# Kernel tuning notes

Measured on AMD Instinct MI355X. Metric: run time of the kernel, lower is better.

## Reference

```python
import jax, jax.numpy as jnp
import numpy as np

N = 50000      # nodes
E = 800000     # edges (avg degree 16)
F_IN = 128
H = 128
C = 2
EPS = 1e-5


def setup_inputs() -> dict:
    key = jax.random.key(0)
    ks = jax.random.split(key, 16)
    s_in = 1.0 / np.sqrt(F_IN)
    s_h = 1.0 / np.sqrt(H)
    return {
        "x": jax.random.normal(ks[0], (N, F_IN), jnp.float32),
        "edge_index": jax.random.randint(ks[1], (2, E), 0, N, jnp.int32),
        "W1": jax.random.normal(ks[2], (F_IN, H), jnp.float32) * s_in,
        "b1": jnp.zeros((H,), jnp.float32),
        "g1": jax.random.uniform(ks[3], (H,), jnp.float32, 0.5, 1.5),
        "be1": jnp.zeros((H,), jnp.float32),
        "m1": jax.random.normal(ks[4], (H,), jnp.float32) * 0.1,
        "v1": jax.random.uniform(ks[5], (H,), jnp.float32, 0.5, 1.5),
        "W2": jax.random.normal(ks[6], (H, H), jnp.float32) * s_h,
        "b2": jnp.zeros((H,), jnp.float32),
        "g2": jax.random.uniform(ks[7], (H,), jnp.float32, 0.5, 1.5),
        "be2": jnp.zeros((H,), jnp.float32),
        "m2": jax.random.normal(ks[8], (H,), jnp.float32) * 0.1,
        "v2": jax.random.uniform(ks[9], (H,), jnp.float32, 0.5, 1.5),
        "Wc": jax.random.normal(ks[10], (H, C), jnp.float32) * s_h,
        "bc": jnp.zeros((C,), jnp.float32),
    }


def _gcn_norm(edge_index):
    # Add self-loops: A_tilde = A + I, then symmetric normalization D^-1/2 A_tilde D^-1/2.
    loop = jnp.arange(N, dtype=edge_index.dtype)
    src = jnp.concatenate([edge_index[0], loop])
    dst = jnp.concatenate([edge_index[1], loop])
    deg = jax.ops.segment_sum(jnp.ones_like(src, jnp.float32), dst, num_segments=N)
    dinv = jnp.where(deg > 0, jax.lax.rsqrt(jnp.maximum(deg, 1.0)), 0.0)
    norm = dinv[src] * dinv[dst]  # per-edge coefficient
    return src, dst, norm


def _gcn_conv(h, src, dst, norm, W, b):
    h = h @ W                                  # [N, H]
    msg = h[src] * norm[:, None]               # gather + scale, [E+N, H]
    out = jax.ops.segment_sum(msg, dst, num_segments=N)
    return out + b


def _bn_eval(h, g, be, m, v):
    return (h - m) * (g * jax.lax.rsqrt(v + EPS)) + be


def reference(x, edge_index, W1, b1, g1, be1, m1, v1,
              W2, b2, g2, be2, m2, v2, Wc, bc):
    src, dst, norm = _gcn_norm(edge_index)
    h = _gcn_conv(x, src, dst, norm, W1, b1)
    h = jax.nn.relu(_bn_eval(h, g1, be1, m1, v1))  # dropout is identity in eval
    h = _gcn_conv(h, src, dst, norm, W2, b2)
    h = jax.nn.relu(_bn_eval(h, g2, be2, m2, v2))
    return h @ Wc + bc                            # logits [N, 2]
```

## Files before the change

kernel.cpp:

```cpp
#include <hip/hip_runtime.h>
#include <hip/hip_fp16.h>

#define EPSV 1e-5f
#define HSZ 6400
#define BPB 32

using half8 = __attribute__((ext_vector_type(8))) _Float16;
using f32x4 = __attribute__((ext_vector_type(4))) float;

__device__ __forceinline__ int bin_lo(int b, int mul) {
    return (int)((((long long)b << 25) + mul - 1) / mul);
}

__global__ __launch_bounds__(128) void k_setup(const float* __restrict__ W1, const float* __restrict__ W2,
                                               _Float16* __restrict__ whi1, _Float16* __restrict__ wlo1,
                                               _Float16* __restrict__ whi2, _Float16* __restrict__ wlo2,
                                               const float* __restrict__ g1, const float* __restrict__ v1,
                                               const float* __restrict__ b1, const float* __restrict__ m1,
                                               const float* __restrict__ be1,
                                               const float* __restrict__ g2, const float* __restrict__ v2,
                                               const float* __restrict__ b2, const float* __restrict__ m2,
                                               const float* __restrict__ be2,
                                               float* __restrict__ par, int* __restrict__ bcur) {
    int b = blockIdx.x;
    int t = threadIdx.x;
    if (b < 32) {
        const float* W = (b < 16) ? W1 : W2;
        _Float16* whi = (b < 16) ? whi1 : whi2;
        _Float16* wlo = (b < 16) ? wlo1 : wlo2;
        int tile = ((b & 15) << 1) | (t >> 6);
        int l = t & 63;
        int kt = tile >> 3, ct = tile & 7;
        int k0 = kt * 32 + (l >> 4) * 8;
        int c = ct * 16 + (l & 15);
        half8 hi, lo;
#pragma unroll
        for (int j = 0; j < 8; j++) {
            float w = W[(k0 + j) * 128 + c];
            _Float16 h = (_Float16)w;
            hi[j] = h;
            lo[j] = (_Float16)(w - (float)h);
        }
        size_t o = (size_t)tile * 64 + l;
        ((half8*)whi)[o] = hi;
        ((half8*)wlo)[o] = lo;
    } else {
        int c = t;
        float s1 = g1[c] * rsqrtf(v1[c] + EPSV);
        par[c] = s1;
        par[128 + c] = fmaf(b1[c] - m1[c], s1, be1[c]);
        float s2 = g2[c] * rsqrtf(v2[c] + EPSV);
        par[256 + c] = s2;
        par[384 + c] = fmaf(b2[c] - m2[c], s2, be2[c]);
        if (c < 8) bcur[c] = 0;
    }
}

__device__ __forceinline__ void bin_body(const int* __restrict__ src, const int* __restrict__ dst,
                                         int* __restrict__ bcur, unsigned int* __restrict__ binned,
                                         int E, int mul, int bin_cap, int bid, int nblocks, int tid) {
    int lane = tid & 63;
    int gw = (bid * 256 + tid) >> 6;
    int nw = (nblocks * 256) >> 6;
    bool v4 = ((E & 3) == 0);
    for (int base = gw * 1024; base < E; base += nw * 1024) {
        unsigned int vals[16];
        int bins[16];
        unsigned long long clo = 0, chi = 0;
#pragma unroll
        for (int g = 0; g < 4; g++) {
            int e0 = base + g * 256 + lane * 4;
            int4 s4, d4;
            if (v4 && e0 + 3 < E) {
                s4 = *(const int4*)(src + e0);
                d4 = *(const int4*)(dst + e0);
            } else {
                s4.x = (e0 < E) ? src[e0] : 0;         d4.x = (e0 < E) ? dst[e0] : -1;
                s4.y = (e0 + 1 < E) ? src[e0 + 1] : 0; d4.y = (e0 + 1 < E) ? dst[e0 + 1] : -1;
                s4.z = (e0 + 2 < E) ? src[e0 + 2] : 0; d4.z = (e0 + 2 < E) ? dst[e0 + 2] : -1;
                s4.w = (e0 + 3 < E) ? src[e0 + 3] : 0; d4.w = (e0 + 3 < E) ? dst[e0 + 3] : -1;
            }
            int ss[4] = {s4.x, s4.y, s4.z, s4.w};
            int dd[4] = {d4.x, d4.y, d4.z, d4.w};
#pragma unroll
            for (int k = 0; k < 4; k++) {
                int j = g * 4 + k;
                int d = dd[k];
                if (d >= 0) {
                    vals[j] = ((unsigned int)ss[k] << 16) | (unsigned int)d;
                    int b = (d * mul) >> 25;
                    bins[j] = b;
                    if (b < 4) clo += 1ull << (b * 16);
                    else       chi += 1ull << ((b - 4) * 16);
                } else bins[j] = -1;
            }
        }
        unsigned long long ilo = clo, ihi = chi;
#pragma unroll
        for (int d = 1; d < 64; d <<= 1) {
            unsigned long long ulo = __shfl_up(ilo, d, 64);
            unsigned long long uhi = __shfl_up(ihi, d, 64);
            if (lane >= d) { ilo += ulo; ihi += uhi; }
        }
        unsigned long long tlo = __shfl(ilo, 63, 64), thi = __shfl(ihi, 63, 64);
        unsigned long long plo = ilo - clo, phi = ihi - chi;
        int mytot = 0;
        if (lane < 4) mytot = (int)((tlo >> (lane * 16)) & 0xffff);
        else if (lane < 8) mytot = (int)((thi >> ((lane - 4) * 16)) & 0xffff);
        int alloc = 0;
        if (lane < 8) alloc = atomicAdd(&bcur[lane], mytot);
#pragma unroll
        for (int j = 0; j < 16; j++) {
            int b = bins[j];
            int bs = (b < 0) ? 0 : b;
            int bbase = __shfl(alloc, bs, 64);
            int sh = (bs & 3) * 16;
            unsigned long long sel = (bs < 4) ? plo : phi;
            int rel = (int)((sel >> sh) & 0xffffu);
            unsigned long long inc = 1ull << sh;
            if (bs < 4) plo += inc; else phi += inc;
            if (b >= 0) binned[(size_t)bs * bin_cap + bbase + rel] = vals[j];
        }
    }
}

template <bool AFP16>
__device__ __forceinline__ void gemm_body(const void* __restrict__ Araw,
                                          const _Float16* __restrict__ whi,
                                          const _Float16* __restrict__ wlo,
                                          unsigned short* __restrict__ out, int M,
                                          int bid, int tid, uint4* __restrict__ sB) {
    int l = tid & 63;
    int w = tid >> 6;
    int r0 = bid * 64 + w * 16;
    int ra = r0 + (l & 15);
    if (ra >= M) ra = M - 1;
    int kl = (l >> 4) * 8;

    half8 avh[4];
    float4 af0[4], af1[4];
    if constexpr (AFP16) {
#pragma unroll
        for (int kt = 0; kt < 4; kt++)
            avh[kt] = *(const half8*)((const _Float16*)Araw + (size_t)ra * 128 + kt * 32 + kl);
    } else {
#pragma unroll
        for (int kt = 0; kt < 4; kt++) {
            const float* pa = (const float*)Araw + (size_t)ra * 128 + kt * 32 + kl;
            af0[kt] = *(const float4*)pa;
            af1[kt] = *(const float4*)(pa + 4);
        }
    }

    {
        const uint4* gh = (const uint4*)whi;
        const uint4* gl = (const uint4*)wlo;
#pragma unroll
        for (int i = 0; i < 8; i++) sB[tid + i * 256] = gh[tid + i * 256];
#pragma unroll
        for (int i = 0; i < 8; i++) sB[2048 + tid + i * 256] = gl[tid + i * 256];
    }
    __syncthreads();

    f32x4 acc[8];
#pragma unroll
    for (int i = 0; i < 8; i++) acc[i] = (f32x4)0.f;

    const half8* bh8 = (const half8*)sB;
    const half8* bl8 = (const half8*)(sB + 2048);

#pragma unroll
    for (int kt = 0; kt < 4; kt++) {
        half8 ah, al;
        if constexpr (AFP16) {
            ah = avh[kt];
        } else {
            float fa[8] = {af0[kt].x, af0[kt].y, af0[kt].z, af0[kt].w,
                           af1[kt].x, af1[kt].y, af1[kt].z, af1[kt].w};
#pragma unroll
            for (int j = 0; j < 8; j++) {
                _Float16 h = (_Float16)fa[j];
                ah[j] = h;
                al[j] = (_Float16)(fa[j] - (float)h);
            }
        }
#pragma unroll
        for (int ct = 0; ct < 8; ct++) {
            half8 bh = bh8[(kt * 8 + ct) * 64 + l];
            half8 bl = bl8[(kt * 8 + ct) * 64 + l];
            acc[ct] = __builtin_amdgcn_mfma_f32_16x16x32_f16(ah, bh, acc[ct], 0, 0, 0);
            if constexpr (!AFP16)
                acc[ct] = __builtin_amdgcn_mfma_f32_16x16x32_f16(al, bh, acc[ct], 0, 0, 0);
            acc[ct] = __builtin_amdgcn_mfma_f32_16x16x32_f16(ah, bl, acc[ct], 0, 0, 0);
        }
    }

    __syncthreads();
    _Float16* stw = (_Float16*)sB + w * 2048;
#pragma unroll
    for (int r = 0; r < 4; r++) {
        int trow = (l >> 4) * 4 + r;
#pragma unroll
        for (int ct = 0; ct < 8; ct++)
            stw[trow * 128 + ct * 16 + (l & 15)] = (_Float16)(acc[ct][r]);
    }
#pragma unroll
    for (int p = 0; p < 4; p++) {
        int trow = p * 4 + (l >> 4);
        int grow = r0 + trow;
        if (grow < M) {
            uint4 v = *(const uint4*)&stw[trow * 128 + (l & 15) * 8];
            *(uint4*)&out[(size_t)grow * 128 + (l & 15) * 8] = v;
        }
    }
}

__global__ __launch_bounds__(256) void k_bingemm(const int* __restrict__ src, const int* __restrict__ dst,
                                                 int* __restrict__ bcur, unsigned int* __restrict__ binned,
                                                 int E, int mul, int bin_cap,
                                                 const float* __restrict__ x,
                                                 const _Float16* __restrict__ whi,
                                                 const _Float16* __restrict__ wlo,
                                                 unsigned short* __restrict__ outHs, int M, int bin_blocks) {
    __shared__ uint4 sB[4096];
    if ((int)blockIdx.x < bin_blocks) {
        bin_body(src, dst, bcur, binned, E, mul, bin_cap, blockIdx.x, bin_blocks, threadIdx.x);
        return;
    }
    gemm_body<false>(x, whi, wlo, outHs, M, blockIdx.x - bin_blocks, threadIdx.x, sB);
}

template <bool AFP16>
__global__ __launch_bounds__(256) void k_gemm(const void* __restrict__ Araw,
                                              const _Float16* __restrict__ whi,
                                              const _Float16* __restrict__ wlo,
                                              unsigned short* __restrict__ out, int M) {
    __shared__ uint4 sB[4096];
    gemm_body<AFP16>(Araw, whi, wlo, out, M, blockIdx.x, threadIdx.x, sB);
}

__global__ __launch_bounds__(256) void k_count(const unsigned int* __restrict__ binned,
                                               const int* __restrict__ bcnt, int* __restrict__ phist,
                                               int mul, int bin_cap) {
    __shared__ int hist[HSZ];
    int b = blockIdx.x & 7;
    int blk = blockIdx.x >> 3;
    int t = threadIdx.x;
    for (int i = t; i < HSZ; i += 256) hist[i] = 0;
    __syncthreads();
    int lo = bin_lo(b, mul);
    int cnt = bcnt[b];
    int e0 = (int)((long long)blk * cnt / BPB);
    int e1 = (int)((long long)(blk + 1) * cnt / BPB);
    const unsigned int* bp = binned + (size_t)b * bin_cap;
    for (int i = e0 + t; i < e1; i += 256) {
        int d = (int)(bp[i] & 0xffffu);
        atomicAdd(&hist[d - lo], 1);
    }
    __syncthreads();
    int* ph = phist + (size_t)blockIdx.x * HSZ;
    for (int i = t; i < HSZ; i += 256) ph[i] = hist[i];
}

__global__ __launch_bounds__(256) void k_bsum(int* __restrict__ phist, int* __restrict__ deg,
                                              int* __restrict__ bsum, int N, int mul) {
    int t = threadIdx.x;
    int base = blockIdx.x * 1024;
    int s = 0;
    for (int j = 0; j < 4; j++) {
        int i = base + j * 256 + t;
        if (i < N) {
            int b = (i * mul) >> 25;
            int lo = bin_lo(b, mul);
            int local = i - lo;
            int run = 0;
#pragma unroll
            for (int blk = 0; blk < BPB; blk++) {
                int* p = phist + (size_t)(blk * 8 + b) * HSZ + local;
                int c = *p;
                *p = run;
                run += c;
            }
            deg[i] = run;
            s += (run + 7) & ~7;
        }
    }
#pragma unroll
    for (int d = 1; d < 64; d <<= 1) s += __shfl_xor(s, d, 64);
    __shared__ int ws[4];
    if ((t & 63) == 0) ws[t >> 6] = s;
    __syncthreads();
    if (t == 0) bsum[blockIdx.x] = ws[0] + ws[1] + ws[2] + ws[3];
}

__global__ __launch_bounds__(256) void k_scanout(const int* __restrict__ deg, const int* __restrict__ bsum,
                                                 int* __restrict__ row_start, int* __restrict__ rend,
                                                 float* __restrict__ dinv, int n, int nb) {
    __shared__ int s_boff;
    __shared__ int ws[4];
    int t = threadIdx.x, lane = t & 63, wid = t >> 6;
    if (t < 64) {
        int v = (t < nb) ? bsum[t] : 0;
        int incl = v;
#pragma unroll
        for (int d = 1; d < 64; d <<= 1) {
            int u = __shfl_up(incl, d, 64);
            if (t >= d) incl += u;
        }
        if (t == (int)blockIdx.x) s_boff = incl - v;
    }
    __syncthreads();
    int base = blockIdx.x * 1024 + t * 4;
    int v[4], pv[4], ts = 0;
#pragma unroll
    for (int j = 0; j < 4; j++) {
        v[j] = (base + j < n) ? deg[base + j] : 0;
        pv[j] = (v[j] + 7) & ~7;
        ts += pv[j];
    }
    int incl = ts;
#pragma unroll
    for (int d = 1; d < 64; d <<= 1) {
        int u = __shfl_up(incl, d, 64);
        if (lane >= d) incl += u;
    }
    if (lane == 63) ws[wid] = incl;
    __syncthreads();
    int wo = 0;
    for (int i = 0; i < wid; i++) wo += ws[i];
    int run = s_boff + wo + (incl - ts);
#pragma unroll
    for (int j = 0; j < 4; j++) {
        if (base + j < n) {
            row_start[base + j] = run;
            rend[base + j] = run + v[j];
            dinv[base + j] = rsqrtf((float)v[j] + 1.0f);
            run += pv[j];
        }
    }
}

__global__ __launch_bounds__(256) void k_fill(const unsigned int* __restrict__ binned,
                                              const int* __restrict__ bcnt, const int* __restrict__ row_start,
                                              const int* __restrict__ phist, const float* __restrict__ dinv,
                                              unsigned int* __restrict__ csr,
                                              int N, int mul, int bin_cap) {
    __shared__ int cur[HSZ];
    int b = blockIdx.x & 7;
    int blk = blockIdx.x >> 3;
    int t = threadIdx.x;
    int lo = bin_lo(b, mul);
    int hi = (b == 7) ? N : bin_lo(b + 1, mul);
    if (hi > N) hi = N;
    const int* ph = phist + (size_t)blockIdx.x * HSZ;
    for (int i = t; i < HSZ; i += 256) {
        int d = lo + i;
        cur[i] = (d < hi) ? (row_start[d] + ph[i]) : 0;
    }
    __syncthreads();
    int cnt = bcnt[b];
    int e0 = (int)((long long)blk * cnt / BPB);
    int e1 = (int)((long long)(blk + 1) * cnt / BPB);
    const unsigned int* bp = binned + (size_t)b * bin_cap;
    for (int i = e0 + t; i < e1; i += 256) {
        unsigned int v = bp[i];
        int d = (int)(v & 0xffffu);
        int s = (int)(v >> 16);
        __half h = __float2half_rn(dinv[s]);
        unsigned short hb = *(unsigned short*)&h;
        int q = atomicAdd(&cur[d - lo], 1);
        csr[q] = ((unsigned int)hb << 16) | (unsigned int)s;
    }
}

__device__ __forceinline__ void f2fma(float2& a, const __half2 h, float w) {
    float2 f = __half22float2(h);
    a.x = fmaf(f.x, w, a.x);
    a.y = fmaf(f.y, w, a.y);
}

__device__ __forceinline__ float pk_w(unsigned int pk) {
    __half h;
    *(unsigned short*)&h = (unsigned short)(pk >> 16);
    return __half2float(h);
}

__device__ __forceinline__ void aggr_gather(const float4* __restrict__ Hs4, const unsigned int* __restrict__ csr,
                                            int rs, int re, int node, float dn, int lc, float2 acc[4]) {
    {
        float4 sv = Hs4[(size_t)node * 16 + lc];
        const __half2* h = (const __half2*)&sv;
        float2 f0 = __half22float2(h[0]), f1 = __half22float2(h[1]);
        float2 f2 = __half22float2(h[2]), f3 = __half22float2(h[3]);
        acc[0] = make_float2(f0.x * dn, f0.y * dn);
        acc[1] = make_float2(f1.x * dn, f1.y * dn);
        acc[2] = make_float2(f2.x * dn, f2.y * dn);
        acc[3] = make_float2(f3.x * dn, f3.y * dn);
    }
    int nch = (re - rs + 7) >> 3;
    if (nch <= 0) return;
    float2 accB[4] = {{0.f, 0.f}, {0.f, 0.f}, {0.f, 0.f}, {0.f, 0.f}};
    const uint4* cp = (const uint4*)(csr + rs);
    uint4 q0 = cp[0], q1 = cp[1];
    for (int c = 0; c < nch; c++) {
        uint4 n0 = q0, n1 = q1;
        if (c + 1 < nch) { n0 = cp[2 * c + 2]; n1 = cp[2 * c + 3]; }
        unsigned int pks[8] = {q0.x, q0.y, q0.z, q0.w, q1.x, q1.y, q1.z, q1.w};
        int base = rs + c * 8;
        float4 v[8];
        float w[8];
#pragma unroll
        for (int j = 0; j < 8; j++) {
            unsigned int pk = (base + j < re) ? pks[j] : 0u;
            int ix = (int)(pk & 0xffffu);
            w[j] = pk_w(pk);
            v[j] = Hs4[(size_t)ix * 16 + lc];
        }
#pragma unroll
        for (int j = 0; j < 8; j++) {
            const __half2* h = (const __half2*)&v[j];
            float2* acp = (j & 1) ? accB : acc;
            f2fma(acp[0], h[0], w[j]);
            f2fma(acp[1], h[1], w[j]);
            f2fma(acp[2], h[2], w[j]);
            f2fma(acp[3], h[3], w[j]);
        }
        q0 = n0; q1 = n1;
    }
#pragma unroll
    for (int k = 0; k < 4; k++) {
        acc[k].x += accB[k].x;
        acc[k].y += accB[k].y;
    }
}

__device__ __forceinline__ void bn_relu(const float2 acc[4], float dn, const float* __restrict__ par,
                                        int lc, float4& y0, float4& y1) {
    float4 s0 = ((const float4*)par)[lc * 2];
    float4 s1 = ((const float4*)par)[lc * 2 + 1];
    float4 t0 = ((const float4*)par)[32 + lc * 2];
    float4 t1 = ((const float4*)par)[32 + lc * 2 + 1];
    y0.x = fmaxf(fmaf(acc[0].x * dn, s0.x, t0.x), 0.f);
    y0.y = fmaxf(fmaf(acc[0].y * dn, s0.y, t0.y), 0.f);
    y0.z = fmaxf(fmaf(acc[1].x * dn, s0.z, t0.z), 0.f);
    y0.w = fmaxf(fmaf(acc[1].y * dn, s0.w, t0.w), 0.f);
    y1.x = fmaxf(fmaf(acc[2].x * dn, s1.x, t1.x), 0.f);
    y1.y = fmaxf(fmaf(acc[2].y * dn, s1.y, t1.y), 0.f);
    y1.z = fmaxf(fmaf(acc[3].x * dn, s1.z, t1.z), 0.f);
    y1.w = fmaxf(fmaf(acc[3].y * dn, s1.w, t1.w), 0.f);
}

__global__ __launch_bounds__(256) void k_aggr(const float4* __restrict__ Hs4, const int* __restrict__ row_start,
                                              const int* __restrict__ rend,
                                              const unsigned int* __restrict__ csr, const float* __restrict__ dinv,
                                              const float* __restrict__ par, uint4* __restrict__ out, int n) {
    int lc = threadIdx.x & 15;
    int node = blockIdx.x * 16 + (threadIdx.x >> 4);
    if (node >= n) return;
    float dn = dinv[node];
    float2 acc[4];
    aggr_gather(Hs4, csr, row_start[node], rend[node], node, dn, lc, acc);
    float4 y0, y1;
    bn_relu(acc, dn, par, lc, y0, y1);
    __half2 p0 = __floats2half2_rn(y0.x, y0.y);
    __half2 p1 = __floats2half2_rn(y0.z, y0.w);
    __half2 p2 = __floats2half2_rn(y1.x, y1.y);
    __half2 p3 = __floats2half2_rn(y1.z, y1.w);
    uint4 pk;
    pk.x = *(unsigned int*)&p0;
    pk.y = *(unsigned int*)&p1;
    pk.z = *(unsigned int*)&p2;
    pk.w = *(unsigned int*)&p3;
    out[(size_t)node * 16 + lc] = pk;
}

__global__ __launch_bounds__(256) void k_aggr_cls(const float4* __restrict__ Hs4, const int* __restrict__ row_start,
                                                  const int* __restrict__ rend,
                                                  const unsigned int* __restrict__ csr, const float* __restrict__ dinv,
                                                  const float* __restrict__ par, const float4* __restrict__ Wc4,
                                                  const float* __restrict__ bc, float2* __restrict__ out, int n) {
    int lc = threadIdx.x & 15;
    int node = blockIdx.x * 16 + (threadIdx.x >> 4);
    if (node >= n) return;
    float dn = dinv[node];
    float2 acc[4];
    aggr_gather(Hs4, csr, row_start[node], rend[node], node, dn, lc, acc);
    float4 y0, y1;
    bn_relu(acc, dn, par, lc, y0, y1);
    float4 w0 = Wc4[lc * 4], w1 = Wc4[lc * 4 + 1], w2 = Wc4[lc * 4 + 2], w3 = Wc4[lc * 4 + 3];
    float p0 = y0.x * w0.x + y0.y * w0.z + y0.z * w1.x + y0.w * w1.z
             + y1.x * w2.x + y1.y * w2.z + y1.z * w3.x + y1.w * w3.z;
    float p1 = y0.x * w0.y + y0.y * w0.w + y0.z * w1.y + y0.w * w1.w
             + y1.x * w2.y + y1.y * w2.w + y1.z * w3.y + y1.w * w3.w;
#pragma unroll
    for (int d = 1; d < 16; d <<= 1) {
        p0 += __shfl_xor(p0, d, 16);
        p1 += __shfl_xor(p1, d, 16);
    }
    if (lc == 0) out[node] = make_float2(p0 + bc[0], p1 + bc[1]);
}

extern "C" void kernel_launch(void* const* d_in, const int* in_sizes, int n_in,
                              void* d_out, int out_size, void* d_ws, size_t ws_size,
                              hipStream_t stream) {
    const float* x = (const float*)d_in[0];
    const int* ei = (const int*)d_in[1];
    const float* W1 = (const float*)d_in[2];
    const float* b1 = (const float*)d_in[3];
    const float* g1 = (const float*)d_in[4];
    const float* be1 = (const float*)d_in[5];
    const float* m1 = (const float*)d_in[6];
    const float* v1 = (const float*)d_in[7];
    const float* W2 = (const float*)d_in[8];
    const float* b2 = (const float*)d_in[9];
    const float* g2 = (const float*)d_in[10];
    const float* be2 = (const float*)d_in[11];
    const float* m2 = (const float*)d_in[12];
    const float* v2 = (const float*)d_in[13];
    const float* Wc = (const float*)d_in[14];
    const float* bc = (const float*)d_in[15];
    float* out = (float*)d_out;

    const int N = in_sizes[0] / 128;
    const int E = in_sizes[1] / 2;
    const int* src = ei;
    const int* dst = ei + E;

    const int mul = (int)((8LL << 25) / N);
    const int bin_cap = ((E / 8 + 8192 + 63) / 64) * 64;

    int* W = (int*)d_ws;
    size_t off = 0;
    int* deg = W + off; off += N;
    int* bcur = W + off; off += 8;
    int* row_start = W + off; off += (size_t)N + 1;
    int* rend = W + off; off += N;
    float* dinv = (float*)(W + off); off += N;
    int* bsum = W + off; off += 64;
    float* par = (float*)(W + off); off += 512;
    _Float16* whi1 = (_Float16*)(W + off); off += 8192;
    _Float16* wlo1 = (_Float16*)(W + off); off += 8192;
    _Float16* whi2 = (_Float16*)(W + off); off += 8192;
    _Float16* wlo2 = (_Float16*)(W + off); off += 8192;
    int* phist = W + off; off += (size_t)8 * BPB * HSZ;
    unsigned int* csr = (unsigned int*)(W + off); off += (size_t)E + 8 * N + 64;
    unsigned int* binned = (unsigned int*)(W + off); off += (size_t)8 * bin_cap;
    off = (off + 3) & ~(size_t)3;
    __half* Hs = (__half*)(W + off); off += (size_t)N * 64;
    _Float16* Ag = (_Float16*)(W + off);

    k_setup<<<33, 128, 0, stream>>>(W1, W2, whi1, wlo1, whi2, wlo2,
                                    g1, v1, b1, m1, be1, g2, v2, b2, m2, be2,
                                    par, bcur);

    int nb = (N + 1023) / 1024;
    int gbm = (N + 63) / 64;
    int bin_blocks = 512;
    k_bingemm<<<bin_blocks + gbm, 256, 0, stream>>>(src, dst, bcur, binned, E, mul, bin_cap,
                                                    x, whi1, wlo1, (unsigned short*)Hs, N, bin_blocks);
    k_count<<<8 * BPB, 256, 0, stream>>>(binned, bcur, phist, mul, bin_cap);
    k_bsum<<<nb, 256, 0, stream>>>(phist, deg, bsum, N, mul);
    k_scanout<<<nb, 256, 0, stream>>>(deg, bsum, row_start, rend, dinv, N, nb);
    k_fill<<<8 * BPB, 256, 0, stream>>>(binned, bcur, row_start, phist, dinv, csr, N, mul, bin_cap);

    int ab = (N + 15) / 16;
    k_aggr<<<ab, 256, 0, stream>>>((const float4*)Hs, row_start, rend, csr, dinv, par, (uint4*)Ag, N);
    k_gemm<true><<<gbm, 256, 0, stream>>>(Ag, whi2, wlo2, (unsigned short*)Hs, N);
    k_aggr_cls<<<ab, 256, 0, stream>>>((const float4*)Hs, row_start, rend, csr, dinv, par + 256,
                                       (const float4*)Wc, bc, (float2*)out, N);
}
```

Measured before the change: 150.7 us.

## Fuse CSR build kernels with grid barriers and unroll aggregation by two chunks

Merges the count, block-sum, scan and fill kernels into one persistent kernel of 256 blocks, separated by atomic-counter grid barriers, to remove three launch gaps. The barrier counter lives in the workspace and is reset by the setup kernel. The aggregation loop now processes two 8-edge chunks per iteration so more gathers are in flight. The spin barrier depends on all 256 blocks being resident at once, and the wider unroll raises register pressure. The unrolled loop also reads csr entries past a row's end, which is only safe if rows are padded to 16 rather than 8.

```diff
diff --git a/kernel.cpp b/kernel.cpp
--- a/kernel.cpp
+++ b/kernel.cpp
@@ -52,7 +52,7 @@
         float s2 = g2[c] * rsqrtf(v2[c] + EPSV);
         par[256 + c] = s2;
         par[384 + c] = fmaf(b2[c] - m2[c], s2, be2[c]);
-        if (c < 8) bcur[c] = 0;
+        if (c < 9) bcur[c] = 0;
     }
 }
 
@@ -239,137 +239,139 @@
     gemm_body<AFP16>(Araw, whi, wlo, out, M, blockIdx.x, threadIdx.x, sB);
 }
 
-__global__ __launch_bounds__(256) void k_count(const unsigned int* __restrict__ binned,
-                                               const int* __restrict__ bcnt, int* __restrict__ phist,
-                                               int mul, int bin_cap) {
-    __shared__ int hist[HSZ];
-    int b = blockIdx.x & 7;
-    int blk = blockIdx.x >> 3;
+__device__ __forceinline__ void gbar(int* __restrict__ cnt, int target) {
+    __syncthreads();
+    if (threadIdx.x == 0) {
+        __threadfence();
+        atomicAdd(cnt, 1);
+        while (atomicAdd(cnt, 0) < target) { }
+        __threadfence();
+    }
+    __syncthreads();
+}
+
+__global__ __launch_bounds__(256) void k_csr(const unsigned int* __restrict__ binned,
+                                             const int* __restrict__ bcnt, int* __restrict__ phist,
+                                             int* __restrict__ deg, int* __restrict__ bsum,
+                                             int* __restrict__ row_start, int* __restrict__ rend,
+                                             float* __restrict__ dinv, unsigned int* __restrict__ csr,
+                                             int* __restrict__ barcnt,
+                                             int N, int mul, int bin_cap, int nb) {
+    __shared__ int lds[HSZ];
+    int bid = blockIdx.x;
     int t = threadIdx.x;
-    for (int i = t; i < HSZ; i += 256) hist[i] = 0;
-    __syncthreads();
+    int b = bid & 7;
+    int blk = bid >> 3;
     int lo = bin_lo(b, mul);
     int cnt = bcnt[b];
     int e0 = (int)((long long)blk * cnt / BPB);
     int e1 = (int)((long long)(blk + 1) * cnt / BPB);
     const unsigned int* bp = binned + (size_t)b * bin_cap;
+
+    for (int i = t; i < HSZ; i += 256) lds[i] = 0;
+    __syncthreads();
     for (int i = e0 + t; i < e1; i += 256) {
         int d = (int)(bp[i] & 0xffffu);
-        atomicAdd(&hist[d - lo], 1);
+        atomicAdd(&lds[d - lo], 1);
     }
     __syncthreads();
-    int* ph = phist + (size_t)blockIdx.x * HSZ;
-    for (int i = t; i < HSZ; i += 256) ph[i] = hist[i];
-}
-
-__global__ __launch_bounds__(256) void k_bsum(int* __restrict__ phist, int* __restrict__ deg,
-                                              int* __restrict__ bsum, int N, int mul) {
-    int t = threadIdx.x;
-    int base = blockIdx.x * 1024;
-    int s = 0;
-    for (int j = 0; j < 4; j++) {
-        int i = base + j * 256 + t;
-        if (i < N) {
-            int b = (i * mul) >> 25;
-            int lo = bin_lo(b, mul);
-            int local = i - lo;
-            int run = 0;
-#pragma unroll
-            for (int blk = 0; blk < BPB; blk++) {
-                int* p = phist + (size_t)(blk * 8 + b) * HSZ + local;
-                int c = *p;
-                *p = run;
-                run += c;
+    {
+        int* ph = phist + (size_t)bid * HSZ;
+        for (int i = t; i < HSZ; i += 256) ph[i] = lds[i];
+    }
+    gbar(barcnt, 256);
+
+    if (bid < nb) {
+        int base = bid * 1024;
+        int s = 0;
+        for (int j = 0; j < 4; j++) {
+            int i = base + j * 256 + t;
+            if (i < N) {
+                int bb = (i * mul) >> 25;
+                int blo = bin_lo(bb, mul);
+                int local = i - blo;
+                int run = 0;
+#pragma unroll
+                for (int k = 0; k < BPB; k++) {
+                    int* p = phist + (size_t)(k * 8 + bb) * HSZ + local;
+                    int c = *p;
+                    *p = run;
+                    run += c;
+                }
+                deg[i] = run;
+                s += (run + 7) & ~7;
             }
-            deg[i] = run;
-            s += (run + 7) & ~7;
-        }
-    }
-#pragma unroll
-    for (int d = 1; d < 64; d <<= 1) s += __shfl_xor(s, d, 64);
-    __shared__ int ws[4];
-    if ((t & 63) == 0) ws[t >> 6] = s;
-    __syncthreads();
-    if (t == 0) bsum[blockIdx.x] = ws[0] + ws[1] + ws[2] + ws[3];
-}
-
-__global__ __launch_bounds__(256) void k_scanout(const int* __restrict__ deg, const int* __restrict__ bsum,
-                                                 int* __restrict__ row_start, int* __restrict__ rend,
-                                                 float* __restrict__ dinv, int n, int nb) {
-    __shared__ int s_boff;
-    __shared__ int ws[4];
-    int t = threadIdx.x, lane = t & 63, wid = t >> 6;
-    if (t < 64) {
-        int v = (t < nb) ? bsum[t] : 0;
-        int incl = v;
+        }
+#pragma unroll
+        for (int d = 1; d < 64; d <<= 1) s += __shfl_xor(s, d, 64);
+        if ((t & 63) == 0) lds[t >> 6] = s;
+        __syncthreads();
+        if (t == 0) bsum[bid] = lds[0] + lds[1] + lds[2] + lds[3];
+    }
+    gbar(barcnt, 512);
+
+    if (bid < nb) {
+        int lane = t & 63, wid = t >> 6;
+        if (t < 64) {
+            int v = (t < nb) ? bsum[t] : 0;
+            int incl = v;
+#pragma unroll
+            for (int d = 1; d < 64; d <<= 1) {
+                int u = __shfl_up(incl, d, 64);
+                if (t >= d) incl += u;
+            }
+            if (t == bid) lds[4] = incl - v;
+        }
+        __syncthreads();
+        int base = bid * 1024 + t * 4;
+        int v[4], pv[4], ts = 0;
+#pragma unroll
+        for (int j = 0; j < 4; j++) {
+            v[j] = (base + j < N) ? deg[base + j] : 0;
+            pv[j] = (v[j] + 7) & ~7;
+            ts += pv[j];
+        }
+        int incl = ts;
 #pragma unroll
         for (int d = 1; d < 64; d <<= 1) {
             int u = __shfl_up(incl, d, 64);
-            if (t >= d) incl += u;
-        }
-        if (t == (int)blockIdx.x) s_boff = incl - v;
-    }
-    __syncthreads();
-    int base = blockIdx.x * 1024 + t * 4;
-    int v[4], pv[4], ts = 0;
-#pragma unroll
-    for (int j = 0; j < 4; j++) {
-        v[j] = (base + j < n) ? deg[base + j] : 0;
-        pv[j] = (v[j] + 7) & ~7;
-        ts += pv[j];
-    }
-    int incl = ts;
-#pragma unroll
-    for (int d = 1; d < 64; d <<= 1) {
-        int u = __shfl_up(incl, d, 64);
-        if (lane >= d) incl += u;
-    }
-    if (lane == 63) ws[wid] = incl;
-    __syncthreads();
-    int wo = 0;
-    for (int i = 0; i < wid; i++) wo += ws[i];
-    int run = s_boff + wo + (incl - ts);
-#pragma unroll
-    for (int j = 0; j < 4; j++) {
-        if (base + j < n) {
-            row_start[base + j] = run;
-            rend[base + j] = run + v[j];
-            dinv[base + j] = rsqrtf((float)v[j] + 1.0f);
-            run += pv[j];
-        }
-    }
-}
-
-__global__ __launch_bounds__(256) void k_fill(const unsigned int* __restrict__ binned,
-                                              const int* __restrict__ bcnt, const int* __restrict__ row_start,
-                                              const int* __restrict__ phist, const float* __restrict__ dinv,
-                                              unsigned int* __restrict__ csr,
-                                              int N, int mul, int bin_cap) {
-    __shared__ int cur[HSZ];
-    int b = blockIdx.x & 7;
-    int blk = blockIdx.x >> 3;
-    int t = threadIdx.x;
-    int lo = bin_lo(b, mul);
-    int hi = (b == 7) ? N : bin_lo(b + 1, mul);
-    if (hi > N) hi = N;
-    const int* ph = phist + (size_t)blockIdx.x * HSZ;
-    for (int i = t; i < HSZ; i += 256) {
-        int d = lo + i;
-        cur[i] = (d < hi) ? (row_start[d] + ph[i]) : 0;
-    }
-    __syncthreads();
-    int cnt = bcnt[b];
-    int e0 = (int)((long long)blk * cnt / BPB);
-    int e1 = (int)((long long)(blk + 1) * cnt / BPB);
-    const unsigned int* bp = binned + (size_t)b * bin_cap;
-    for (int i = e0 + t; i < e1; i += 256) {
-        unsigned int v = bp[i];
-        int d = (int)(v & 0xffffu);
-        int s = (int)(v >> 16);
-        __half h = __float2half_rn(dinv[s]);
-        unsigned short hb = *(unsigned short*)&h;
-        int q = atomicAdd(&cur[d - lo], 1);
-        csr[q] = ((unsigned int)hb << 16) | (unsigned int)s;
+            if (lane >= d) incl += u;
+        }
+        if (lane == 63) lds[wid] = incl;
+        __syncthreads();
+        int wo = 0;
+        for (int i = 0; i < wid; i++) wo += lds[i];
+        int run = lds[4] + wo + (incl - ts);
+#pragma unroll
+        for (int j = 0; j < 4; j++) {
+            if (base + j < N) {
+                row_start[base + j] = run;
+                rend[base + j] = run + v[j];
+                dinv[base + j] = rsqrtf((float)v[j] + 1.0f);
+                run += pv[j];
+            }
+        }
+    }
+    gbar(barcnt, 768);
+
+    {
+        int hi = (b == 7) ? N : bin_lo(b + 1, mul);
+        if (hi > N) hi = N;
+        const int* ph = phist + (size_t)bid * HSZ;
+        for (int i = t; i < HSZ; i += 256) {
+            int d = lo + i;
+            lds[i] = (d < hi) ? (row_start[d] + ph[i]) : 0;
+        }
+        __syncthreads();
+        for (int i = e0 + t; i < e1; i += 256) {
+            unsigned int v = bp[i];
+            int d = (int)(v & 0xffffu);
+            int s = (int)(v >> 16);
+            __half h = __float2half_rn(dinv[s]);
+            unsigned short hb = *(unsigned short*)&h;
+            int q = atomicAdd(&lds[d - lo], 1);
+            csr[q] = ((unsigned int)hb << 16) | (unsigned int)s;
+        }
     }
 }
 
@@ -401,31 +403,48 @@
     if (nch <= 0) return;
     float2 accB[4] = {{0.f, 0.f}, {0.f, 0.f}, {0.f, 0.f}, {0.f, 0.f}};
     const uint4* cp = (const uint4*)(csr + rs);
-    uint4 q0 = cp[0], q1 = cp[1];
-    for (int c = 0; c < nch; c++) {
-        uint4 n0 = q0, n1 = q1;
-        if (c + 1 < nch) { n0 = cp[2 * c + 2]; n1 = cp[2 * c + 3]; }
-        unsigned int pks[8] = {q0.x, q0.y, q0.z, q0.w, q1.x, q1.y, q1.z, q1.w};
-        int base = rs + c * 8;
-        float4 v[8];
-        float w[8];
+    uint4 qa0 = cp[0], qa1 = cp[1];
+    uint4 qb0 = cp[2], qb1 = cp[3];
+    for (int c = 0; c < nch; c += 2) {
+        uint4 na0 = qa0, na1 = qa1, nb0 = qb0, nb1 = qb1;
+        if (c + 2 < nch) { na0 = cp[2 * c + 4]; na1 = cp[2 * c + 5]; nb0 = cp[2 * c + 6]; nb1 = cp[2 * c + 7]; }
+        unsigned int pA[8] = {qa0.x, qa0.y, qa0.z, qa0.w, qa1.x, qa1.y, qa1.z, qa1.w};
+        unsigned int pB[8] = {qb0.x, qb0.y, qb0.z, qb0.w, qb1.x, qb1.y, qb1.z, qb1.w};
+        int baseA = rs + c * 8;
+        int baseB = baseA + 8;
+        float4 vA[8], vB[8];
+        float wA[8], wB[8];
 #pragma unroll
         for (int j = 0; j < 8; j++) {
-            unsigned int pk = (base + j < re) ? pks[j] : 0u;
-            int ix = (int)(pk & 0xffffu);
-            w[j] = pk_w(pk);
-            v[j] = Hs4[(size_t)ix * 16 + lc];
+            unsigned int pk = (baseA + j < re) ? pA[j] : 0u;
+            wA[j] = pk_w(pk);
+            vA[j] = Hs4[(size_t)(pk & 0xffffu) * 16 + lc];
         }
 #pragma unroll
         for (int j = 0; j < 8; j++) {
-            const __half2* h = (const __half2*)&v[j];
+            unsigned int pk = (baseB + j < re) ? pB[j] : 0u;
+            wB[j] = pk_w(pk);
+            vB[j] = Hs4[(size_t)(pk & 0xffffu) * 16 + lc];
+        }
+#pragma unroll
+        for (int j = 0; j < 8; j++) {
+            const __half2* h = (const __half2*)&vA[j];
             float2* acp = (j & 1) ? accB : acc;
-            f2fma(acp[0], h[0], w[j]);
-            f2fma(acp[1], h[1], w[j]);
-            f2fma(acp[2], h[2], w[j]);
-            f2fma(acp[3], h[3], w[j]);
-        }
-        q0 = n0; q1 = n1;
+            f2fma(acp[0], h[0], wA[j]);
+            f2fma(acp[1], h[1], wA[j]);
+            f2fma(acp[2], h[2], wA[j]);
+            f2fma(acp[3], h[3], wA[j]);
+        }
+#pragma unroll
+        for (int j = 0; j < 8; j++) {
+            const __half2* h = (const __half2*)&vB[j];
+            float2* acp = (j & 1) ? accB : acc;
+            f2fma(acp[0], h[0], wB[j]);
+            f2fma(acp[1], h[1], wB[j]);
+            f2fma(acp[2], h[2], wB[j]);
+            f2fma(acp[3], h[3], wB[j]);
+        }
+        qa0 = na0; qa1 = na1; qb0 = nb0; qb1 = nb1;
     }
 #pragma unroll
     for (int k = 0; k < 4; k++) {
@@ -532,7 +551,7 @@
     int* W = (int*)d_ws;
     size_t off = 0;
     int* deg = W + off; off += N;
-    int* bcur = W + off; off += 8;
+    int* bcur = W + off; off += 9;
     int* row_start = W + off; off += (size_t)N + 1;
     int* rend = W + off; off += N;
     float* dinv = (float*)(W + off); off += N;
@@ -558,10 +577,8 @@
     int bin_blocks = 512;
     k_bingemm<<<bin_blocks + gbm, 256, 0, stream>>>(src, dst, bcur, binned, E, mul, bin_cap,
                                                     x, whi1, wlo1, (unsigned short*)Hs, N, bin_blocks);
-    k_count<<<8 * BPB, 256, 0, stream>>>(binned, bcur, phist, mul, bin_cap);
-    k_bsum<<<nb, 256, 0, stream>>>(phist, deg, bsum, N, mul);
-    k_scanout<<<nb, 256, 0, stream>>>(deg, bsum, row_start, rend, dinv, N, nb);
-    k_fill<<<8 * BPB, 256, 0, stream>>>(binned, bcur, row_start, phist, dinv, csr, N, mul, bin_cap);
+    k_csr<<<8 * BPB, 256, 0, stream>>>(binned, bcur, phist, deg, bsum, row_start, rend, dinv,
+                                       csr, bcur + 8, N, mul, bin_cap, nb);
 
     int ab = (N + 15) / 16;
     k_aggr<<<ab, 256, 0, stream>>>((const float4*)Hs, row_start, rend, csr, dinv, par, (uint4*)Ag, N);
```

Result: slower. 206.1 us (+36.8%).
